# Kernel optimization log

Measured on AMD Instinct MI355X. Metric: run time of the kernel, lower is better.

## Reference

```python
import jax, jax.numpy as jnp
import numpy as np

SCOPE = 63          # length of ricker inhibition filter (odd)
IN_CHANNELS = 256   # circulant matrix size == channel dim
SELF_CONNECT = False


def ricker(scope, width, damp, self_connect=False):
    # symmetric ricker (mexican-hat) wavelet of length `scope`, centered
    x = jnp.arange(scope, dtype=jnp.float32) - scope // 2
    w2 = width * width
    r = damp * (1.0 - x * x / w2) * jnp.exp(-x * x / (2.0 * w2))
    if not self_connect:
        r = r.at[scope // 2].set(0.0)  # no self-connection: zero center tap
    return r


def toeplitz1d_circular(f, size):
    # embed the centered length-`scope` filter into the first row of a
    # size x size circulant matrix (center tap on the diagonal, tails wrap)
    half = f.shape[0] // 2
    row0 = jnp.zeros(size, f.dtype)
    row0 = row0.at[: half + 1].set(f[half:])      # center + right tail
    row0 = row0.at[size - half:].set(f[:half])    # left tail wraps around
    idx = (jnp.arange(size)[:, None] - jnp.arange(size)[None, :]) % size
    return row0[idx]  # C[i, j] = row0[(i - j) mod size]


def setup_inputs() -> dict:
    key = jax.random.key(0)
    activations = jax.random.normal(key, (64, IN_CHANNELS, 56, 56), dtype=jnp.float32)
    damp = jnp.asarray(0.12, dtype=jnp.float32)   # learnable scalar
    width = jnp.asarray(3.0, dtype=jnp.float32)   # learnable scalar
    return {"activations": activations, "damp": damp, "width": width}


def reference(activations, damp, width):
    f = ricker(SCOPE, width, damp, SELF_CONNECT)
    tpl = toeplitz1d_circular(f, IN_CHANNELS)
    tpl_inv = jnp.linalg.inv(jnp.eye(IN_CHANNELS, dtype=f.dtype) - tpl)
    # apply inhibition matrix along the channel axis at every pixel
    return jnp.einsum('ij,bjhw->bihw', tpl_inv, activations)
```

## Files before the change

kernel.cpp:

```cpp
#include <hip/hip_runtime.h>


#define IN_CH 256
#define HW    3136
#define TP    64
#define KS    32

typedef _Float16 f16x8  __attribute__((ext_vector_type(8)));
typedef float    f32x16 __attribute__((ext_vector_type(16)));
typedef unsigned int u32;


__global__ __launch_bounds__(256) void pi_build(const float* __restrict__ damp,
                                                const float* __restrict__ width,
                                                f16x8* __restrict__ afrag) {
    __shared__ float cS[256], gS[256], ctab[256], mS[256];
    int t = threadIdx.x;
    float w = width[0], dmp = damp[0];

    ctab[t] = cosf((float)t * 0.0245436926f );

    int x = (t < 128) ? t : t - 256;
    float cv = 0.0f;
    if (t != 0 && x >= -31 && x <= 31) {
        float fx2 = (float)(x * x);
        float w2  = w * w;
        cv = dmp * (1.0f - fx2 / w2) * expf(-fx2 / (2.0f * w2));
    }
    cS[t] = cv;
    __syncthreads();

    float lam = 0.0f;
#pragma unroll 8
    for (int n = 0; n < 256; n++) lam += cS[n] * ctab[(t * n) & 255];
    gS[t] = 1.0f / (1.0f - lam);
    __syncthreads();

    float md = 0.0f;
#pragma unroll 8
    for (int k = 0; k < 256; k++) md += gS[k] * ctab[(t * k) & 255];
    mS[t] = md * (1.0f / 256.0f);
    __syncthreads();

#pragma unroll
    for (int g = 0; g < 32; g++) {
        int gid = g * 256 + t;
        int l  = gid & 63;
        int tt = (gid >> 6) & 7;
        int s  = gid >> 9;
        int i     = 32 * tt + (l & 31);
        int kbase = 16 * s + 8 * (l >> 5);
        f16x8 h;
#pragma unroll
        for (int j = 0; j < 8; j++)
            h[j] = (_Float16)mS[(i - (kbase + j)) & 255];
        afrag[gid] = h;
    }
}

__device__ __forceinline__ void gl_lds16(const float* g, const float* l) {
    __builtin_amdgcn_global_load_lds(
        (const __attribute__((address_space(1))) u32*)g,
        (__attribute__((address_space(3))) u32*)l, 16, 0, 0);
}

__global__ __launch_bounds__(256, 4) void pi_gemm(const float* __restrict__ act,
                                                  float* __restrict__ out,
                                                  const f16x8* __restrict__ afrag) {
    __shared__ float lds[4][KS][TP];

    int tid  = threadIdx.x;
    int lane = tid & 63;
    int wv   = tid >> 6;

    int b    = blockIdx.x / 49;
    int tile = blockIdx.x - b * 49;
    int p0   = tile * TP;

    const float* actb = act + (size_t)b * (IN_CH * HW) + p0;
    float*       outb = out + (size_t)b * (IN_CH * HW) + p0;

    const float* gsrc = actb + (size_t)(lane >> 4) * HW + (lane & 15) * 4;

    int lo = lane & 31;
    int hi = lane >> 5;

    f32x16 acc[2][2] = {};

#define STAGE(st) do {                                                         \
    gl_lds16(gsrc + (size_t)((st) * KS + 8 * wv    ) * HW,                     \
             &lds[(st) & 3][8 * wv    ][0]);                                   \
    gl_lds16(gsrc + (size_t)((st) * KS + 8 * wv + 4) * HW,                     \
             &lds[(st) & 3][8 * wv + 4][0]);                                   \
} while (0)

#define WAITB(N) do {                                                          \
    __builtin_amdgcn_sched_barrier(0);                                         \
    asm volatile("s_waitcnt vmcnt(" #N ")" ::: "memory");                      \
    __builtin_amdgcn_s_barrier();                                              \
    __builtin_amdgcn_sched_barrier(0);                                         \
} while (0)

#define KSTEP(t) do {                                                          \
    const float (*buf)[TP] = lds[(t) & 3];                                     \
    f16x8 bf0[2], bf1[2];                                                      \
    _Pragma("unroll")                                                          \
    for (int s = 0; s < 2; s++) {                                              \
        _Pragma("unroll")                                                      \
        for (int j = 0; j < 8; j++) {                                          \
            bf0[s][j] = (_Float16)buf[16 * s + 8 * hi + j][lo];                \
            bf1[s][j] = (_Float16)buf[16 * s + 8 * hi + j][32 + lo];           \
        }                                                                      \
    }                                                                          \
    _Pragma("unroll")                                                          \
    for (int s = 0; s < 2; s++) {                                              \
        f16x8 a0 = afrag[((2 * (t) + s) * 8 + 2 * wv    ) * 64 + lane];        \
        f16x8 a1 = afrag[((2 * (t) + s) * 8 + 2 * wv + 1) * 64 + lane];        \
        acc[0][0] = __builtin_amdgcn_mfma_f32_32x32x16_f16(a0, bf0[s], acc[0][0], 0, 0, 0); \
        acc[0][1] = __builtin_amdgcn_mfma_f32_32x32x16_f16(a0, bf1[s], acc[0][1], 0, 0, 0); \
        acc[1][0] = __builtin_amdgcn_mfma_f32_32x32x16_f16(a1, bf0[s], acc[1][0], 0, 0, 0); \
        acc[1][1] = __builtin_amdgcn_mfma_f32_32x32x16_f16(a1, bf1[s], acc[1][1], 0, 0, 0); \
    }                                                                          \
} while (0)

    STAGE(0); STAGE(1); STAGE(2);

    WAITB(4); STAGE(3); KSTEP(0);
    WAITB(4); STAGE(4); KSTEP(1);
    WAITB(4); STAGE(5); KSTEP(2);
    WAITB(4); STAGE(6); KSTEP(3);
    WAITB(4); STAGE(7); KSTEP(4);
    WAITB(4);           KSTEP(5);
    WAITB(2);           KSTEP(6);
    WAITB(0);           KSTEP(7);

#undef STAGE
#undef WAITB
#undef KSTEP

    int rb = 4 * hi;
#pragma unroll
    for (int ti = 0; ti < 2; ti++) {
#pragma unroll
        for (int ni = 0; ni < 2; ni++) {
            float* dst = outb + (size_t)(64 * wv + 32 * ti + rb) * HW + 32 * ni + lo;
#pragma unroll
            for (int r = 0; r < 16; r++) {
                int row = (r & 3) + 8 * (r >> 2);
                __builtin_nontemporal_store(acc[ti][ni][r], dst + (size_t)row * HW);
            }
        }
    }
}

extern "C" void kernel_launch(void* const* d_in, const int* in_sizes, int n_in,
                              void* d_out, int out_size, void* d_ws, size_t ws_size,
                              hipStream_t stream) {
    const float* act   = (const float*)d_in[0];
    const float* damp  = (const float*)d_in[1];
    const float* width = (const float*)d_in[2];
    float* out = (float*)d_out;

    f16x8* afrag = (f16x8*)d_ws;
    int batches = in_sizes[0] / (IN_CH * HW);

    pi_build<<<1, 256, 0, stream>>>(damp, width, afrag);
    pi_gemm<<<batches * 49, 256, 0, stream>>>(act, out, afrag);
}
```

Baseline: 364.5 us.

## Split output channels across two blocks per tile and preload A fragments into registers

Each pixel tile is now handled by two blocks, each computing 128 of the 256 output channels, so the grid doubles and each wave owns one 32-row slice. The wave's A fragments are loaded into registers once before the K loop instead of being fetched from global memory every step. This raises parallelism and lowers accumulator register use. In exchange, each activation tile is read twice, relying on cache to absorb the duplicate traffic.

Measured after the change: 363.8 us. Within noise of the previous version (-0.2%).

```diff
diff --git a/kernel.cpp b/kernel.cpp
--- a/kernel.cpp
+++ b/kernel.cpp
@@ -73,19 +73,28 @@
     int lane = tid & 63;
     int wv   = tid >> 6;
 
-    int b    = blockIdx.x / 49;
-    int tile = blockIdx.x - b * 49;
+    int bid  = blockIdx.x;
+    int h    = bid & 1;
+    int bt   = bid >> 1;
+    int b    = bt / 49;
+    int tile = bt - b * 49;
     int p0   = tile * TP;
+    int t    = 4 * h + wv;
 
     const float* actb = act + (size_t)b * (IN_CH * HW) + p0;
     float*       outb = out + (size_t)b * (IN_CH * HW) + p0;
 
-    const float* gsrc = actb + (size_t)(lane >> 4) * HW + (lane & 15) * 4;
-
     int lo = lane & 31;
     int hi = lane >> 5;
 
-    f32x16 acc[2][2] = {};
+    f16x8 ar[16];
+#pragma unroll
+    for (int s = 0; s < 16; s++)
+        ar[s] = afrag[(s * 8 + t) * 64 + lane];
+
+    const float* gsrc = actb + (size_t)(lane >> 4) * HW + (lane & 15) * 4;
+
+    f32x16 acc[2] = {};
 
 #define STAGE(st) do {                                                         \
     gl_lds16(gsrc + (size_t)((st) * KS + 8 * wv    ) * HW,                     \
@@ -101,25 +110,18 @@
     __builtin_amdgcn_sched_barrier(0);                                         \
 } while (0)
 
-#define KSTEP(t) do {                                                          \
-    const float (*buf)[TP] = lds[(t) & 3];                                     \
-    f16x8 bf0[2], bf1[2];                                                      \
+#define KSTEP(kk) do {                                                         \
+    const float (*buf)[TP] = lds[(kk) & 3];                                    \
     _Pragma("unroll")                                                          \
     for (int s = 0; s < 2; s++) {                                              \
+        f16x8 b0, b1;                                                          \
         _Pragma("unroll")                                                      \
         for (int j = 0; j < 8; j++) {                                          \
-            bf0[s][j] = (_Float16)buf[16 * s + 8 * hi + j][lo];                \
-            bf1[s][j] = (_Float16)buf[16 * s + 8 * hi + j][32 + lo];           \
+            b0[j] = (_Float16)buf[16 * s + 8 * hi + j][lo];                    \
+            b1[j] = (_Float16)buf[16 * s + 8 * hi + j][32 + lo];               \
         }                                                                      \
-    }                                                                          \
-    _Pragma("unroll")                                                          \
-    for (int s = 0; s < 2; s++) {                                              \
-        f16x8 a0 = afrag[((2 * (t) + s) * 8 + 2 * wv    ) * 64 + lane];        \
-        f16x8 a1 = afrag[((2 * (t) + s) * 8 + 2 * wv + 1) * 64 + lane];        \
-        acc[0][0] = __builtin_amdgcn_mfma_f32_32x32x16_f16(a0, bf0[s], acc[0][0], 0, 0, 0); \
-        acc[0][1] = __builtin_amdgcn_mfma_f32_32x32x16_f16(a0, bf1[s], acc[0][1], 0, 0, 0); \
-        acc[1][0] = __builtin_amdgcn_mfma_f32_32x32x16_f16(a1, bf0[s], acc[1][0], 0, 0, 0); \
-        acc[1][1] = __builtin_amdgcn_mfma_f32_32x32x16_f16(a1, bf1[s], acc[1][1], 0, 0, 0); \
+        acc[0] = __builtin_amdgcn_mfma_f32_32x32x16_f16(ar[2 * (kk) + s], b0, acc[0], 0, 0, 0); \
+        acc[1] = __builtin_amdgcn_mfma_f32_32x32x16_f16(ar[2 * (kk) + s], b1, acc[1], 0, 0, 0); \
     }                                                                          \
 } while (0)
 
@@ -140,15 +142,12 @@
 
     int rb = 4 * hi;
 #pragma unroll
-    for (int ti = 0; ti < 2; ti++) {
+    for (int ni = 0; ni < 2; ni++) {
+        float* dst = outb + (size_t)(32 * t + rb) * HW + 32 * ni + lo;
 #pragma unroll
-        for (int ni = 0; ni < 2; ni++) {
-            float* dst = outb + (size_t)(64 * wv + 32 * ti + rb) * HW + 32 * ni + lo;
-#pragma unroll
-            for (int r = 0; r < 16; r++) {
-                int row = (r & 3) + 8 * (r >> 2);
-                __builtin_nontemporal_store(acc[ti][ni][r], dst + (size_t)row * HW);
-            }
+        for (int r = 0; r < 16; r++) {
+            int row = (r & 3) + 8 * (r >> 2);
+            __builtin_nontemporal_store(acc[ni][r], dst + (size_t)row * HW);
         }
     }
 }
@@ -165,5 +164,5 @@
     int batches = in_sizes[0] / (IN_CH * HW);
 
     pi_build<<<1, 256, 0, stream>>>(damp, width, afrag);
-    pi_gemm<<<batches * 49, 256, 0, stream>>>(act, out, afrag);
+    pi_gemm<<<batches * 49 * 2, 256, 0, stream>>>(act, out, afrag);
 }
```
